# Kernel optimization log

Measured on AMD Instinct MI355X. Metric: run time of the kernel, lower is better.

## Reference

```python
import jax, jax.numpy as jnp
import numpy as np

PATTERN = np.array([3, 5, 8, 12, 16, 21, 27, 36], dtype=np.int64)
REPEATS = 32
GROUPS = np.tile(PATTERN, REPEATS)   # 256 ragged group sizes
G = int(GROUPS.size)                 # 256 groups
F = int(GROUPS.sum())                # 4096 total features
B = 8192
SPLIT = G - 3                        # split_idx = num_groups - 3
H1, H2 = 512, 256
EPS = 1e-5


def _xavier(key, shape):
    fan_in, fan_out = shape
    lim = float(np.sqrt(6.0 / (fan_in + fan_out)))
    return jax.random.uniform(key, shape, jnp.float32, -lim, lim)


def setup_inputs() -> dict:
    key = jax.random.key(0)
    ks = jax.random.split(key, 8)
    # segment id for every feature column -> its gene group
    seg = jnp.asarray(np.repeat(np.arange(G), GROUPS), dtype=jnp.int32)
    x = jax.random.normal(ks[0], (B, F), jnp.float32)
    # per-group Linear(group,1) weights, flattened; xavier limit per group size
    lims = np.sqrt(6.0 / (GROUPS + 1.0))
    w_gene = jax.random.uniform(ks[1], (F,), jnp.float32, -1.0, 1.0) * jnp.asarray(np.repeat(lims, GROUPS), jnp.float32)
    return {
        "x": x, "seg": seg,
        "w_gene": w_gene, "b_gene": jnp.zeros((G,), jnp.float32),
        "W1g1": _xavier(ks[2], (SPLIT, H1)), "b1g1": jnp.zeros((H1,), jnp.float32),
        "W2g1": _xavier(ks[3], (H1, H2)), "b2g1": jnp.zeros((H2,), jnp.float32),
        "W1g2": _xavier(ks[4], (3, H1)), "b1g2": jnp.zeros((H1,), jnp.float32),
        "W2g2": _xavier(ks[5], (H1, H2)), "b2g2": jnp.zeros((H2,), jnp.float32),
        "gamma1g1": jnp.ones((H1,), jnp.float32), "beta1g1": jnp.zeros((H1,), jnp.float32),
        "gamma2g1": jnp.ones((H2,), jnp.float32), "beta2g1": jnp.zeros((H2,), jnp.float32),
        "gamma1g2": jnp.ones((H1,), jnp.float32), "beta1g2": jnp.zeros((H1,), jnp.float32),
        "gamma2g2": jnp.ones((H2,), jnp.float32), "beta2g2": jnp.zeros((H2,), jnp.float32),
        "W_out": _xavier(ks[6], (2 * H2, 1)), "b_out": jnp.zeros((1,), jnp.float32),
        "W_res": _xavier(ks[7], (G, 1)), "b_res": jnp.zeros((1,), jnp.float32),
    }


def _bn(h, gamma, beta):
    # BatchNorm1d in training mode: biased batch statistics over the batch axis
    mu = jnp.mean(h, axis=0)
    var = jnp.var(h, axis=0)
    return (h - mu) * jax.lax.rsqrt(var + EPS) * gamma + beta


def reference(x, seg, w_gene, b_gene, W1g1, b1g1, W2g1, b2g1, W1g2, b1g2, W2g2, b2g2,
              gamma1g1, beta1g1, gamma2g1, beta2g1, gamma1g2, beta1g2, gamma2g2, beta2g2,
              W_out, b_out, W_res, b_res):
    # The loop of tiny Linear(group,1)+ReLU over contiguous feature slices is
    # exactly a ragged weighted segment-sum: [B, F] -> [B, G]
    gene = jax.nn.relu(jax.ops.segment_sum((x * w_gene).T, seg, num_segments=G).T + b_gene)
    g1, g2 = gene[:, :SPLIT], gene[:, SPLIT:]
    # dropout p = 0.0 -> identity
    h1 = jax.nn.relu(_bn(g1 @ W1g1 + b1g1, gamma1g1, beta1g1))
    h1 = jax.nn.relu(_bn(h1 @ W2g1 + b2g1, gamma2g1, beta2g1))
    h2 = jax.nn.relu(_bn(g2 @ W1g2 + b1g2, gamma1g2, beta1g2))
    h2 = jax.nn.relu(_bn(h2 @ W2g2 + b2g2, gamma2g2, beta2g2))
    combined = jnp.concatenate([h1, h2], axis=1)           # [B, 2*H2]
    return combined @ W_out + b_out + gene @ W_res + b_res  # [B, 1]
```

## Files before the change

### kernel.cpp

```cpp
#include <hip/hip_runtime.h>
#include <cstddef>

#define BATCH  8192
#define NFEAT  4096
#define NGRP   256
#define NSPLIT 253
#define NH1    512
#define NH2    256
#define EPSV   1e-5f

typedef __bf16 bf16_8 __attribute__((ext_vector_type(8)));
typedef float  f32x4  __attribute__((ext_vector_type(4)));

__constant__ int c_prefix[8] = {0,3,8,16,28,44,65,92};
__constant__ int c_gsize[8]  = {3,5,8,12,16,21,27,36};

__global__ __launch_bounds__(256) void gene_kernel(const float* __restrict__ x,
        const float* __restrict__ wg, const float* __restrict__ bg,
        __bf16* __restrict__ geneb)
{
    __shared__ float prod[NFEAT + 32 * 8];
    __shared__ float gout[NGRP];
    int t = threadIdx.x;
    size_t row = blockIdx.x;
    const float4* xv = (const float4*)(x + row * NFEAT);
    const float4* wv = (const float4*)wg;
#pragma unroll
    for (int i = 0; i < 4; i++) {
        int idx = t + 256 * i;
        float4 a = xv[idx], w = wv[idx];
        float4 p; p.x = a.x*w.x; p.y = a.y*w.y; p.z = a.z*w.z; p.w = a.w*w.w;
        int f = idx * 4;
        *(float4*)&prod[f + ((f >> 7) << 3)] = p;
    }
    __syncthreads();
    int sub = t & 7, gidx = t >> 3;
    int gi  = gidx & 7, fbo = gidx >> 3;
    int pre = c_prefix[gi], len = c_gsize[gi];
#pragma unroll
    for (int s = 0; s < 8; s++) {
        int base = (4 * s + fbo) * 136 + pre;
        float v = 0.f;
        for (int j = sub; j < len; j += 8) v += prod[base + j];
        v += __shfl_down(v, 4, 8);
        v += __shfl_down(v, 2, 8);
        v += __shfl_down(v, 1, 8);
        if (sub == 0) gout[(s << 5) + gidx] = v;
    }
    __syncthreads();
    geneb[row * NGRP + t] = (__bf16)fmaxf(gout[t] + bg[t], 0.f);
}

__global__ __launch_bounds__(256) void transpose_all(
        const float* __restrict__ W1g1, const float* __restrict__ W2g1,
        const float* __restrict__ W2g2,
        __bf16* __restrict__ w1t, __bf16* __restrict__ w2at, __bf16* __restrict__ w2bt)
{
    __shared__ float tile[32][33];
    int z = blockIdx.z;
    const float* src; __bf16* dst; int K, N, Kp;
    if (z == 0)      { src = W1g1; dst = w1t;  K = NSPLIT; N = NH1; Kp = 256; }
    else if (z == 1) { src = W2g1; dst = w2at; K = NH1;    N = NH2; Kp = NH1; }
    else             { src = W2g2; dst = w2bt; K = NH1;    N = NH2; Kp = NH1; }
    int ktiles = (K + 31) >> 5, ntiles = N >> 5;
    int tid = blockIdx.y * 16 + blockIdx.x;
    if (tid >= ktiles * ntiles) return;
    int kt = (tid % ktiles) * 32, nt = (tid / ktiles) * 32;
    int tx = threadIdx.x & 31, ty = threadIdx.x >> 5;
    for (int r = ty; r < 32; r += 8) {
        int k = kt + r, n = nt + tx;
        tile[r][tx] = (k < K && n < N) ? src[(size_t)k * N + n] : 0.f;
    }
    __syncthreads();
    for (int r = ty; r < 32; r += 8) {
        int n = nt + r, k = kt + tx;
        if (n < N && k < Kp) dst[(size_t)n * Kp + k] = (__bf16)tile[tx][r];
    }
}

__global__ __launch_bounds__(256) void gemm1_fused(
    const __bf16* __restrict__ geneb, const __bf16* __restrict__ w1t,
    const float* __restrict__ b1g1, __bf16* __restrict__ h1pre,
    float* __restrict__ s1a, float* __restrict__ q1a,
    const float* __restrict__ W1g2, const float* __restrict__ b1g2,
    __bf16* __restrict__ bufA, float* __restrict__ s2a, float* __restrict__ q2a)
{
    __shared__ __align__(16) char smem[19456];
    int t = threadIdx.x;

    if (blockIdx.x == 8) {
        float* Ws  = (float*)smem;
        float* bsh = Ws + 1536;
        float* gv  = bsh + 512;
        for (int i = t; i < 1536; i += 256) Ws[i] = W1g2[i];
        for (int i = t; i < 512; i += 256) bsh[i] = b1g2[i];
        int row0 = blockIdx.y * 64;
        if (t < 192)
            gv[t] = (float)geneb[(size_t)(row0 + t / 3) * NGRP + NSPLIT + (t % 3)];
        __syncthreads();
        int c0 = t, c1 = t + 256;
        float s0 = 0, q0 = 0, s1 = 0, q1 = 0;
        for (int r = 0; r < 64; r++) {
            float a = gv[3 * r], b = gv[3 * r + 1], c = gv[3 * r + 2];
            float v0 = bsh[c0] + a * Ws[c0] + b * Ws[512 + c0] + c * Ws[1024 + c0];
            float v1 = bsh[c1] + a * Ws[c1] + b * Ws[512 + c1] + c * Ws[1024 + c1];
            size_t base = (size_t)(row0 + r) * NH1;
            bufA[base + c0] = (__bf16)v0; bufA[base + c1] = (__bf16)v1;
            s0 += v0; q0 += v0 * v0; s1 += v1; q1 += v1 * v1;
        }
        atomicAdd(&s2a[c0], s0); atomicAdd(&q2a[c0], q0);
        atomicAdd(&s2a[c1], s1); atomicAdd(&q2a[c1], q1);
        return;
    }

    const int K = 256;
    __bf16 (*As)[72] = (__bf16(*)[72])smem;
    __bf16 (*Bs)[72] = (__bf16(*)[72])(smem + 9216);
    float* sred = (float*)(smem + 18432);
    float* qred = sred + 64;

    int n0 = blockIdx.x * 64;
    int m0 = blockIdx.y * 64;
    if (t < 64) { sred[t] = 0.f; qred[t] = 0.f; }

    int lane = t & 63, w = t >> 6;
    int wm = (w & 1) * 32, wn = (w >> 1) * 32;
    int fm = lane & 15, quad = lane >> 4;

    f32x4 acc[2][2];
#pragma unroll
    for (int i = 0; i < 2; i++)
#pragma unroll
        for (int j = 0; j < 2; j++) acc[i][j] = (f32x4){0.f, 0.f, 0.f, 0.f};

    int r0 = t >> 3;
    int kc = (t & 7) * 8;

    for (int kt = 0; kt < (K >> 6); kt++) {
        int kk = kt << 6;
        __syncthreads();
#pragma unroll
        for (int h = 0; h < 2; h++) {
            int row = r0 + h * 32;
            *(uint4*)&As[row][kc] = *(const uint4*)(geneb + (size_t)(m0 + row) * NGRP + kk + kc);
            *(uint4*)&Bs[row][kc] = *(const uint4*)(w1t + (size_t)(n0 + row) * K + kk + kc);
        }
        __syncthreads();
#pragma unroll
        for (int kc2 = 0; kc2 < 64; kc2 += 32) {
            bf16_8 a0 = *(const bf16_8*)&As[wm + fm][kc2 + quad * 8];
            bf16_8 a1 = *(const bf16_8*)&As[wm + 16 + fm][kc2 + quad * 8];
            bf16_8 b0 = *(const bf16_8*)&Bs[wn + fm][kc2 + quad * 8];
            bf16_8 b1 = *(const bf16_8*)&Bs[wn + 16 + fm][kc2 + quad * 8];
            acc[0][0] = __builtin_amdgcn_mfma_f32_16x16x32_bf16(a0, b0, acc[0][0], 0, 0, 0);
            acc[0][1] = __builtin_amdgcn_mfma_f32_16x16x32_bf16(a0, b1, acc[0][1], 0, 0, 0);
            acc[1][0] = __builtin_amdgcn_mfma_f32_16x16x32_bf16(a1, b0, acc[1][0], 0, 0, 0);
            acc[1][1] = __builtin_amdgcn_mfma_f32_16x16x32_bf16(a1, b1, acc[1][1], 0, 0, 0);
        }
    }

    float myS[2] = {0.f, 0.f}, myQ[2] = {0.f, 0.f};
#pragma unroll
    for (int j = 0; j < 2; j++) {
        int col = n0 + wn + j * 16 + fm;
        float bv = b1g1[col];
#pragma unroll
        for (int i = 0; i < 2; i++)
#pragma unroll
            for (int r = 0; r < 4; r++) {
                float v = acc[i][j][r] + bv;
                int row = m0 + wm + i * 16 + quad * 4 + r;
                h1pre[(size_t)row * NH1 + col] = (__bf16)v;
                myS[j] += v; myQ[j] += v * v;
            }
    }
#pragma unroll
    for (int j = 0; j < 2; j++) {
        atomicAdd(&sred[wn + j * 16 + fm], myS[j]);
        atomicAdd(&qred[wn + j * 16 + fm], myQ[j]);
    }
    __syncthreads();
    if (t < 64) {
        atomicAdd(&s1a[n0 + t], sred[t]);
        atomicAdd(&q1a[n0 + t], qred[t]);
    }
}

__global__ __launch_bounds__(256) void gemm2_dual(
    const __bf16* A0, const __bf16* A1,
    const __bf16* WT0, const __bf16* WT1,
    const float* bias0, const float* bias1,
    __bf16* C0, __bf16* C1,
    float* csum0, float* csq0, float* csum1, float* csq1,
    const float* as0, const float* aq0, const float* ag0, const float* ab0,
    const float* as1, const float* aq1, const float* ag1, const float* ab1)
{
    const int K = NH1, n_total = NH2;
    __shared__ __align__(16) __bf16 As[64][72];
    __shared__ __align__(16) __bf16 Bs[64][72];
    __shared__ float bnsc[NH1];
    __shared__ float bnsh[NH1];
    __shared__ float sred[64];
    __shared__ float qred[64];

    int z = blockIdx.z;
    const __bf16* A    = z ? A1 : A0;
    const __bf16* WT   = z ? WT1 : WT0;
    const float*  bias = z ? bias1 : bias0;
    __bf16*       C    = z ? C1 : C0;
    float* csum = z ? csum1 : csum0;
    float* csq  = z ? csq1  : csq0;
    const float* a_sum = z ? as1 : as0;
    const float* a_sq  = z ? aq1 : aq0;
    const float* a_g   = z ? ag1 : ag0;
    const float* a_b   = z ? ab1 : ab0;

    int t = threadIdx.x;
    int n0 = blockIdx.x * 64;
    int m0 = blockIdx.y * 64;
    {
        const float invB = 1.f / (float)BATCH;
        for (int k = t; k < K; k += 256) {
            float mu  = a_sum[k] * invB;
            float var = a_sq[k] * invB - mu * mu;
            float sc  = a_g[k] * rsqrtf(var + EPSV);
            bnsc[k] = sc;
            bnsh[k] = a_b[k] - mu * sc;
        }
    }
    if (t < 64) { sred[t] = 0.f; qred[t] = 0.f; }

    int lane = t & 63, w = t >> 6;
    int wm = (w & 1) * 32, wn = (w >> 1) * 32;
    int fm = lane & 15, quad = lane >> 4;

    f32x4 acc[2][2];
#pragma unroll
    for (int i = 0; i < 2; i++)
#pragma unroll
        for (int j = 0; j < 2; j++) acc[i][j] = (f32x4){0.f, 0.f, 0.f, 0.f};

    int r0 = t >> 3;
    int kc = (t & 7) * 8;

    for (int kt = 0; kt < (K >> 6); kt++) {
        int kk = kt << 6;
        __syncthreads();
#pragma unroll
        for (int h = 0; h < 2; h++) {
            int row = r0 + h * 32;
            uint4 raw = *(const uint4*)(A + (size_t)(m0 + row) * K + kk + kc);
            __bf16 vals[8];
#pragma unroll
            for (int c = 0; c < 4; c++) {
                unsigned uu = (&raw.x)[c];
                int kg = kk + kc + 2 * c;
                float flo = __uint_as_float(uu << 16);
                float fhi = __uint_as_float(uu & 0xffff0000u);
                flo = fmaxf(fmaf(flo, bnsc[kg],     bnsh[kg]),     0.f);
                fhi = fmaxf(fmaf(fhi, bnsc[kg + 1], bnsh[kg + 1]), 0.f);
                vals[2 * c]     = (__bf16)flo;
                vals[2 * c + 1] = (__bf16)fhi;
            }
            *(bf16_8*)&As[row][kc] = *(bf16_8*)vals;
            *(uint4*)&Bs[row][kc] = *(const uint4*)(WT + (size_t)(n0 + row) * K + kk + kc);
        }
        __syncthreads();
#pragma unroll
        for (int kc2 = 0; kc2 < 64; kc2 += 32) {
            bf16_8 a0 = *(const bf16_8*)&As[wm + fm][kc2 + quad * 8];
            bf16_8 a1 = *(const bf16_8*)&As[wm + 16 + fm][kc2 + quad * 8];
            bf16_8 b0 = *(const bf16_8*)&Bs[wn + fm][kc2 + quad * 8];
            bf16_8 b1 = *(const bf16_8*)&Bs[wn + 16 + fm][kc2 + quad * 8];
            acc[0][0] = __builtin_amdgcn_mfma_f32_16x16x32_bf16(a0, b0, acc[0][0], 0, 0, 0);
            acc[0][1] = __builtin_amdgcn_mfma_f32_16x16x32_bf16(a0, b1, acc[0][1], 0, 0, 0);
            acc[1][0] = __builtin_amdgcn_mfma_f32_16x16x32_bf16(a1, b0, acc[1][0], 0, 0, 0);
            acc[1][1] = __builtin_amdgcn_mfma_f32_16x16x32_bf16(a1, b1, acc[1][1], 0, 0, 0);
        }
    }

    float myS[2] = {0.f, 0.f}, myQ[2] = {0.f, 0.f};
#pragma unroll
    for (int j = 0; j < 2; j++) {
        int col = n0 + wn + j * 16 + fm;
        float bv = bias[col];
#pragma unroll
        for (int i = 0; i < 2; i++)
#pragma unroll
            for (int r = 0; r < 4; r++) {
                float v = acc[i][j][r] + bv;
                int row = m0 + wm + i * 16 + quad * 4 + r;
                C[(size_t)row * n_total + col] = (__bf16)v;
                myS[j] += v; myQ[j] += v * v;
            }
    }
#pragma unroll
    for (int j = 0; j < 2; j++) {
        atomicAdd(&sred[wn + j * 16 + fm], myS[j]);
        atomicAdd(&qred[wn + j * 16 + fm], myQ[j]);
    }
    __syncthreads();
    if (t < 64) {
        atomicAdd(&csum[n0 + t], sred[t]);
        atomicAdd(&csq[n0 + t], qred[t]);
    }
}

__global__ __launch_bounds__(256) void final_kernel(
    const __bf16* __restrict__ h1, const __bf16* __restrict__ h2,
    const __bf16* __restrict__ geneb,
    const float* __restrict__ s1, const float* __restrict__ q1,
    const float* __restrict__ gm1, const float* __restrict__ bt1,
    const float* __restrict__ s2, const float* __restrict__ q2,
    const float* __restrict__ gm2, const float* __restrict__ bt2,
    const float* __restrict__ Wout, const float* __restrict__ bo,
    const float* __restrict__ Wres, const float* __restrict__ br,
    float* __restrict__ outp)
{
    int t = threadIdx.x, lane = t & 63, wv = t >> 6;
    int row = blockIdx.x * 4 + wv;
    int c = lane * 4;
    const float invB = 1.f / (float)BATCH;
    float4 vs1 = *(const float4*)&s1[c],  vq1 = *(const float4*)&q1[c];
    float4 vg1 = *(const float4*)&gm1[c], vb1 = *(const float4*)&bt1[c];
    float4 vs2 = *(const float4*)&s2[c],  vq2 = *(const float4*)&q2[c];
    float4 vg2 = *(const float4*)&gm2[c], vb2 = *(const float4*)&bt2[c];
    float4 wo1 = *(const float4*)&Wout[c];
    float4 wo2 = *(const float4*)&Wout[NH2 + c];
    float4 wr  = *(const float4*)&Wres[c];
    ushort4 u1 = *(const ushort4*)((const unsigned short*)h1 + (size_t)row * NH2 + c);
    ushort4 u2 = *(const ushort4*)((const unsigned short*)h2 + (size_t)row * NH2 + c);
    ushort4 ug = *(const ushort4*)((const unsigned short*)geneb + (size_t)row * NGRP + c);
    float acc = 0.f;
#pragma unroll
    for (int e = 0; e < 4; e++) {
        float h1f = __uint_as_float((unsigned)(&u1.x)[e] << 16);
        float h2f = __uint_as_float((unsigned)(&u2.x)[e] << 16);
        float gvf = __uint_as_float((unsigned)(&ug.x)[e] << 16);
        float mu  = (&vs1.x)[e] * invB;
        float var = (&vq1.x)[e] * invB - mu * mu;
        float v   = (h1f - mu) * (&vg1.x)[e] * rsqrtf(var + EPSV) + (&vb1.x)[e];
        acc += fmaxf(v, 0.f) * (&wo1.x)[e];
        mu  = (&vs2.x)[e] * invB;
        var = (&vq2.x)[e] * invB - mu * mu;
        v   = (h2f - mu) * (&vg2.x)[e] * rsqrtf(var + EPSV) + (&vb2.x)[e];
        acc += fmaxf(v, 0.f) * (&wo2.x)[e];
        acc += gvf * (&wr.x)[e];
    }
#pragma unroll
    for (int off = 32; off > 0; off >>= 1) acc += __shfl_down(acc, off, 64);
    if (lane == 0) outp[row] = acc + bo[0] + br[0];
}

extern "C" void kernel_launch(void* const* d_in, const int* in_sizes, int n_in,
                              void* d_out, int out_size, void* d_ws, size_t ws_size,
                              hipStream_t stream)
{
    (void)in_sizes; (void)n_in; (void)out_size; (void)ws_size;
    const float* x        = (const float*)d_in[0];
    const float* wgene    = (const float*)d_in[2];
    const float* bgene    = (const float*)d_in[3];
    const float* W1g1     = (const float*)d_in[4];
    const float* b1g1     = (const float*)d_in[5];
    const float* W2g1     = (const float*)d_in[6];
    const float* b2g1     = (const float*)d_in[7];
    const float* W1g2     = (const float*)d_in[8];
    const float* b1g2     = (const float*)d_in[9];
    const float* W2g2     = (const float*)d_in[10];
    const float* b2g2     = (const float*)d_in[11];
    const float* gamma1g1 = (const float*)d_in[12];
    const float* beta1g1  = (const float*)d_in[13];
    const float* gamma2g1 = (const float*)d_in[14];
    const float* beta2g1  = (const float*)d_in[15];
    const float* gamma1g2 = (const float*)d_in[16];
    const float* beta1g2  = (const float*)d_in[17];
    const float* gamma2g2 = (const float*)d_in[18];
    const float* beta2g2  = (const float*)d_in[19];
    const float* Wout     = (const float*)d_in[20];
    const float* bout     = (const float*)d_in[21];
    const float* Wres     = (const float*)d_in[22];
    const float* bres     = (const float*)d_in[23];
    float* outp = (float*)d_out;

    char* p = (char*)d_ws;
    __bf16* geneb = (__bf16*)p;           p += (size_t)BATCH * NGRP * 2;
    __bf16* h1pre = (__bf16*)p;           p += (size_t)BATCH * NH1 * 2;
    __bf16* bufA  = (__bf16*)p;           p += (size_t)BATCH * NH1 * 2;
    __bf16* h1b   = (__bf16*)p;           p += (size_t)BATCH * NH2 * 2;
    __bf16* h2b   = (__bf16*)p;           p += (size_t)BATCH * NH2 * 2;
    __bf16* w1t   = (__bf16*)p;           p += (size_t)NH1 * 256 * 2;
    __bf16* w2at  = (__bf16*)p;           p += (size_t)NH2 * NH1 * 2;
    __bf16* w2bt  = (__bf16*)p;           p += (size_t)NH2 * NH1 * 2;
    float*  st    = (float*)p;
    float* s1a = st;          float* q1a = st + 512;
    float* s1b = st + 1024;   float* q1b = st + 1536;
    float* s2a = st + 2048;   float* q2a = st + 2560;
    float* s2b = st + 3072;   float* q2b = st + 3584;

    hipMemsetAsync(st, 0, 4096 * sizeof(float), stream);

    transpose_all<<<dim3(16, 16, 3), 256, 0, stream>>>(W1g1, W2g1, W2g2, w1t, w2at, w2bt);

    gene_kernel<<<BATCH, 256, 0, stream>>>(x, wgene, bgene, geneb);

    gemm1_fused<<<dim3(9, BATCH / 64), 256, 0, stream>>>(
        geneb, w1t, b1g1, h1pre, s1a, q1a,
        W1g2, b1g2, bufA, s2a, q2a);

    gemm2_dual<<<dim3(NH2 / 64, BATCH / 64, 2), 256, 0, stream>>>(
        h1pre, bufA, w2at, w2bt, b2g1, b2g2, h1b, h2b,
        s1b, q1b, s2b, q2b,
        s1a, q1a, gamma1g1, beta1g1,
        s2a, q2a, gamma1g2, beta1g2);

    final_kernel<<<BATCH / 4, 256, 0, stream>>>(
        h1b, h2b, geneb,
        s1b, q1b, gamma2g1, beta2g1,
        s2b, q2b, gamma2g2, beta2g2,
        Wout, bout, Wres, bres, outp);
}
```

Baseline: 277.4 us.

## Fold memset and weight transposes into gene kernel; batch final rows per wave

The memset of the BN statistics buffer and the three weight transposes now run as extra blocks inside the gene segment-sum kernel, which removes two launches and a memset from the stream. The gene kernel now writes its bf16 output as 16-byte vectors from 32 threads instead of scalar stores. The final kernel precomputes the BN scale and shift once per thread and handles two rows per wave, halving the grid and reusing the parameter loads. Mixing transpose blocks into the large gene grid adds some divergence in block roles.

Result: no change. 273.5 us (-1.4%).

```diff
diff --git a/kernel.cpp b/kernel.cpp
--- a/kernel.cpp
+++ b/kernel.cpp
@@ -15,14 +15,51 @@
 __constant__ int c_prefix[8] = {0,3,8,16,28,44,65,92};
 __constant__ int c_gsize[8]  = {3,5,8,12,16,21,27,36};
 
-__global__ __launch_bounds__(256) void gene_kernel(const float* __restrict__ x,
-        const float* __restrict__ wg, const float* __restrict__ bg,
-        __bf16* __restrict__ geneb)
+__global__ __launch_bounds__(256) void gene_aux_kernel(
+        const float* __restrict__ x, const float* __restrict__ wg,
+        const float* __restrict__ bg, __bf16* __restrict__ geneb,
+        const float* __restrict__ W1g1, const float* __restrict__ W2g1,
+        const float* __restrict__ W2g2,
+        __bf16* __restrict__ w1t, __bf16* __restrict__ w2at, __bf16* __restrict__ w2bt,
+        float* __restrict__ st)
 {
-    __shared__ float prod[NFEAT + 32 * 8];
-    __shared__ float gout[NGRP];
+    __shared__ __align__(16) char smem[(NFEAT + 32 * 8) * 4 + NGRP * 4];
     int t = threadIdx.x;
-    size_t row = blockIdx.x;
+    int bid = blockIdx.x;
+
+    if (bid >= 8192) {
+        int j = bid - 8192;
+        if (j == 384) {
+            float4 z = {0.f, 0.f, 0.f, 0.f};
+#pragma unroll
+            for (int i = 0; i < 4; i++) *(float4*)&st[(t + 256 * i) * 4] = z;
+            return;
+        }
+        float (*tile)[33] = (float(*)[33])smem;
+        int z = j >> 7, tid = j & 127;
+        const float* src; __bf16* dst; int K, N, Kp;
+        if (z == 0)      { src = W1g1; dst = w1t;  K = NSPLIT; N = NH1; Kp = 256; }
+        else if (z == 1) { src = W2g1; dst = w2at; K = NH1;    N = NH2; Kp = NH1; }
+        else             { src = W2g2; dst = w2bt; K = NH1;    N = NH2; Kp = NH1; }
+        int ktiles = (K + 31) >> 5;
+        if (tid >= ktiles * (N >> 5)) return;
+        int kt = (tid % ktiles) * 32, nt = (tid / ktiles) * 32;
+        int tx = t & 31, ty = t >> 5;
+        for (int r = ty; r < 32; r += 8) {
+            int k = kt + r, n = nt + tx;
+            tile[r][tx] = (k < K && n < N) ? src[(size_t)k * N + n] : 0.f;
+        }
+        __syncthreads();
+        for (int r = ty; r < 32; r += 8) {
+            int n = nt + r, k = kt + tx;
+            if (n < N && k < Kp) dst[(size_t)n * Kp + k] = (__bf16)tile[tx][r];
+        }
+        return;
+    }
+
+    float* prod = (float*)smem;
+    float* gout = prod + NFEAT + 32 * 8;
+    size_t row = bid;
     const float4* xv = (const float4*)(x + row * NFEAT);
     const float4* wv = (const float4*)wg;
 #pragma unroll
@@ -48,33 +85,15 @@
         if (sub == 0) gout[(s << 5) + gidx] = v;
     }
     __syncthreads();
-    geneb[row * NGRP + t] = (__bf16)fmaxf(gout[t] + bg[t], 0.f);
-}
-
-__global__ __launch_bounds__(256) void transpose_all(
-        const float* __restrict__ W1g1, const float* __restrict__ W2g1,
-        const float* __restrict__ W2g2,
-        __bf16* __restrict__ w1t, __bf16* __restrict__ w2at, __bf16* __restrict__ w2bt)
-{
-    __shared__ float tile[32][33];
-    int z = blockIdx.z;
-    const float* src; __bf16* dst; int K, N, Kp;
-    if (z == 0)      { src = W1g1; dst = w1t;  K = NSPLIT; N = NH1; Kp = 256; }
-    else if (z == 1) { src = W2g1; dst = w2at; K = NH1;    N = NH2; Kp = NH1; }
-    else             { src = W2g2; dst = w2bt; K = NH1;    N = NH2; Kp = NH1; }
-    int ktiles = (K + 31) >> 5, ntiles = N >> 5;
-    int tid = blockIdx.y * 16 + blockIdx.x;
-    if (tid >= ktiles * ntiles) return;
-    int kt = (tid % ktiles) * 32, nt = (tid / ktiles) * 32;
-    int tx = threadIdx.x & 31, ty = threadIdx.x >> 5;
-    for (int r = ty; r < 32; r += 8) {
-        int k = kt + r, n = nt + tx;
-        tile[r][tx] = (k < K && n < N) ? src[(size_t)k * N + n] : 0.f;
-    }
-    __syncthreads();
-    for (int r = ty; r < 32; r += 8) {
-        int n = nt + r, k = kt + tx;
-        if (n < N && k < Kp) dst[(size_t)n * Kp + k] = (__bf16)tile[tx][r];
+    if (t < 32) {
+        unsigned short up[8];
+#pragma unroll
+        for (int e = 0; e < 8; e++) {
+            int g = t * 8 + e;
+            __bf16 b = (__bf16)fmaxf(gout[g] + bg[g], 0.f);
+            up[e] = *(unsigned short*)&b;
+        }
+        *(uint4*)((unsigned short*)geneb + row * NGRP + t * 8) = *(uint4*)up;
     }
 }
 
@@ -318,7 +337,7 @@
     float* __restrict__ outp)
 {
     int t = threadIdx.x, lane = t & 63, wv = t >> 6;
-    int row = blockIdx.x * 4 + wv;
+    int row0 = blockIdx.x * 8 + wv * 2;
     int c = lane * 4;
     const float invB = 1.f / (float)BATCH;
     float4 vs1 = *(const float4*)&s1[c],  vq1 = *(const float4*)&q1[c];
@@ -328,28 +347,38 @@
     float4 wo1 = *(const float4*)&Wout[c];
     float4 wo2 = *(const float4*)&Wout[NH2 + c];
     float4 wr  = *(const float4*)&Wres[c];
-    ushort4 u1 = *(const ushort4*)((const unsigned short*)h1 + (size_t)row * NH2 + c);
-    ushort4 u2 = *(const ushort4*)((const unsigned short*)h2 + (size_t)row * NH2 + c);
-    ushort4 ug = *(const ushort4*)((const unsigned short*)geneb + (size_t)row * NGRP + c);
-    float acc = 0.f;
+    float4 sc1, sh1, sc2, sh2;
 #pragma unroll
     for (int e = 0; e < 4; e++) {
-        float h1f = __uint_as_float((unsigned)(&u1.x)[e] << 16);
-        float h2f = __uint_as_float((unsigned)(&u2.x)[e] << 16);
-        float gvf = __uint_as_float((unsigned)(&ug.x)[e] << 16);
         float mu  = (&vs1.x)[e] * invB;
         float var = (&vq1.x)[e] * invB - mu * mu;
-        float v   = (h1f - mu) * (&vg1.x)[e] * rsqrtf(var + EPSV) + (&vb1.x)[e];
-        acc += fmaxf(v, 0.f) * (&wo1.x)[e];
+        float sc  = (&vg1.x)[e] * rsqrtf(var + EPSV);
+        (&sc1.x)[e] = sc; (&sh1.x)[e] = (&vb1.x)[e] - mu * sc;
         mu  = (&vs2.x)[e] * invB;
         var = (&vq2.x)[e] * invB - mu * mu;
-        v   = (h2f - mu) * (&vg2.x)[e] * rsqrtf(var + EPSV) + (&vb2.x)[e];
-        acc += fmaxf(v, 0.f) * (&wo2.x)[e];
-        acc += gvf * (&wr.x)[e];
-    }
-#pragma unroll
-    for (int off = 32; off > 0; off >>= 1) acc += __shfl_down(acc, off, 64);
-    if (lane == 0) outp[row] = acc + bo[0] + br[0];
+        sc  = (&vg2.x)[e] * rsqrtf(var + EPSV);
+        (&sc2.x)[e] = sc; (&sh2.x)[e] = (&vb2.x)[e] - mu * sc;
+    }
+#pragma unroll
+    for (int rr = 0; rr < 2; rr++) {
+        int row = row0 + rr;
+        ushort4 u1 = *(const ushort4*)((const unsigned short*)h1 + (size_t)row * NH2 + c);
+        ushort4 u2 = *(const ushort4*)((const unsigned short*)h2 + (size_t)row * NH2 + c);
+        ushort4 ug = *(const ushort4*)((const unsigned short*)geneb + (size_t)row * NGRP + c);
+        float acc = 0.f;
+#pragma unroll
+        for (int e = 0; e < 4; e++) {
+            float h1f = __uint_as_float((unsigned)(&u1.x)[e] << 16);
+            float h2f = __uint_as_float((unsigned)(&u2.x)[e] << 16);
+            float gvf = __uint_as_float((unsigned)(&ug.x)[e] << 16);
+            acc += fmaxf(fmaf(h1f, (&sc1.x)[e], (&sh1.x)[e]), 0.f) * (&wo1.x)[e];
+            acc += fmaxf(fmaf(h2f, (&sc2.x)[e], (&sh2.x)[e]), 0.f) * (&wo2.x)[e];
+            acc += gvf * (&wr.x)[e];
+        }
+#pragma unroll
+        for (int off = 32; off > 0; off >>= 1) acc += __shfl_down(acc, off, 64);
+        if (lane == 0) outp[row] = acc + bo[0] + br[0];
+    }
 }
 
 extern "C" void kernel_launch(void* const* d_in, const int* in_sizes, int n_in,
@@ -397,11 +426,8 @@
     float* s2a = st + 2048;   float* q2a = st + 2560;
     float* s2b = st + 3072;   float* q2b = st + 3584;
 
-    hipMemsetAsync(st, 0, 4096 * sizeof(float), stream);
-
-    transpose_all<<<dim3(16, 16, 3), 256, 0, stream>>>(W1g1, W2g1, W2g2, w1t, w2at, w2bt);
-
-    gene_kernel<<<BATCH, 256, 0, stream>>>(x, wgene, bgene, geneb);
+    gene_aux_kernel<<<8192 + 384 + 1, 256, 0, stream>>>(
+        x, wgene, bgene, geneb, W1g1, W2g1, W2g2, w1t, w2at, w2bt, st);
 
     gemm1_fused<<<dim3(9, BATCH / 64), 256, 0, stream>>>(
         geneb, w1t, b1g1, h1pre, s1a, q1a,
@@ -413,7 +439,7 @@
         s1a, q1a, gamma1g1, beta1g1,
         s2a, q2a, gamma1g2, beta1g2);
 
-    final_kernel<<<BATCH / 4, 256, 0, stream>>>(
+    final_kernel<<<BATCH / 8, 256, 0, stream>>>(
         h1b, h2b, geneb,
         s1b, q1b, gamma2g1, beta2g1,
         s2b, q2b, gamma2g2, beta2g2,
```
